# Kernel optimization log

Measured on AMD Instinct MI355X. Metric: run time of the kernel, lower is better.

## Reference

```python
import jax, jax.numpy as jnp
import numpy as np

EMB = 1024
FFN = 4096
H = 16
HD = EMB // H
EPS = 1e-6
SLOPE = 0.01


def leaky_relu(x):
    return jnp.where(x >= 0, x, SLOPE * x)


def layer_norm(x, g, b):
    mu = jnp.mean(x, axis=-1, keepdims=True)
    var = jnp.mean((x - mu) ** 2, axis=-1, keepdims=True)
    return (x - mu) * jax.lax.rsqrt(var + EPS) * g + b


def setup_inputs() -> dict:
    key = jax.random.key(0)
    ks = jax.random.split(key, 16)
    B, N = 2, 2048
    x = jax.random.normal(ks[0], (B, N, EMB), dtype=jnp.float32)

    def lin(k, fan_in, fan_out, kaiming_normal):
        kw, kb = jax.random.split(k)
        gain = float(np.sqrt(2.0 / (1.0 + SLOPE ** 2)))
        if kaiming_normal:
            W = jax.random.normal(kw, (fan_out, fan_in)) * (gain / np.sqrt(fan_in))
        else:
            bound = gain * np.sqrt(3.0 / fan_in)
            W = jax.random.uniform(kw, (fan_out, fan_in), minval=-bound, maxval=bound)
        b = jax.random.normal(kb, (fan_out,)) * 1e-6
        return W.astype(jnp.float32), b.astype(jnp.float32)

    Wq, bq = lin(ks[1], EMB, EMB, True)
    Wk, bk = lin(ks[2], EMB, EMB, True)
    Wv, bv = lin(ks[3], EMB, EMB, True)
    Wo, bo = lin(ks[4], EMB, EMB, True)
    W1, b1 = lin(ks[5], EMB, FFN, False)
    W2, b2 = lin(ks[6], FFN, EMB, False)
    return {
        "x": x,
        "ln1_g": jnp.ones((EMB,)), "ln1_b": jnp.zeros((EMB,)),
        "ln2_g": jnp.ones((EMB,)), "ln2_b": jnp.zeros((EMB,)),
        "Wq": Wq, "bq": bq, "Wk": Wk, "bk": bk, "Wv": Wv, "bv": bv,
        "Wo": Wo, "bo": bo, "W1": W1, "b1": b1, "W2": W2, "b2": b2,
    }


def reference(x, ln1_g, ln1_b, ln2_g, ln2_b, Wq, bq, Wk, bk, Wv, bv, Wo, bo, W1, b1, W2, b2):
    B, N, _ = x.shape
    h = x
    xn = layer_norm(x, ln1_g, ln1_b)
    # QKV projections, split heads: [B, H, N, HD]
    def heads(t):
        return t.reshape(B, N, H, HD).transpose(0, 2, 1, 3)
    q = heads(xn @ Wq.T + bq)
    k = heads(xn @ Wk.T + bk)
    v = heads(xn @ Wv.T + bv)
    scores = jnp.einsum('bhnd,bhmd->bhnm', q, k) / jnp.sqrt(jnp.float32(HD))
    probs = leaky_relu(scores)  # non-softmax attention
    ctx = jnp.einsum('bhnm,bhmd->bhnd', probs, v)
    ctx = ctx.transpose(0, 2, 1, 3).reshape(B, N, EMB)
    attn_out = ctx @ Wo.T + bo
    x = attn_out + h
    h = x
    xn = layer_norm(x, ln2_g, ln2_b)
    ff = leaky_relu(xn @ W1.T + b1) @ W2.T + b2
    return ff + h
```

## Files before the change

kernel.cpp:

```cpp
#include <hip/hip_runtime.h>
#include <hip/hip_bf16.h>


typedef unsigned short u16;
typedef unsigned int u32;
typedef __bf16 bf16x8 __attribute__((ext_vector_type(8)));
typedef __bf16 bf16x4 __attribute__((ext_vector_type(4)));
typedef float f32x4 __attribute__((ext_vector_type(4)));
typedef unsigned short u16x8 __attribute__((ext_vector_type(8)));
typedef unsigned int u32x2 __attribute__((ext_vector_type(2)));
typedef short s16x4 __attribute__((ext_vector_type(4)));

typedef const __attribute__((address_space(1))) void* as1cv;
typedef __attribute__((address_space(3))) void* as3v;

#define MFMA16(a, b, c) __builtin_amdgcn_mfma_f32_16x16x32_bf16((a), (b), (c), 0, 0, 0)
#define GLL16(g, l) __builtin_amdgcn_global_load_lds((as1cv)(g), (as3v)(l), 16, 0, 0)

__device__ __forceinline__ u16 f2bf(float f) {
  unsigned u = __builtin_bit_cast(unsigned, f);
  u += 0x7fffu + ((u >> 16) & 1u);
  return (u16)(u >> 16);
}
__device__ __forceinline__ float bf2f(u16 u) {
  return __builtin_bit_cast(float, ((unsigned)u) << 16);
}
__device__ __forceinline__ float lrelu(float v) { return fmaxf(v, 0.01f * v); }

__device__ __forceinline__ void mfma16x16(f32x4& c, bf16x4 a, bf16x4 b) {
#if __has_builtin(__builtin_amdgcn_mfma_f32_16x16x16bf16_1k)
  c = __builtin_amdgcn_mfma_f32_16x16x16bf16_1k(
      __builtin_bit_cast(s16x4, a), __builtin_bit_cast(s16x4, b), c, 0, 0, 0);
#else
  u32x2 au = __builtin_bit_cast(u32x2, a);
  u32x2 bu = __builtin_bit_cast(u32x2, b);
  asm volatile("s_nop 2\n\tv_mfma_f32_16x16x16_bf16 %0, %1, %2, %0"
               : "+v"(c) : "v"(au), "v"(bu));
#endif
}

__device__ __forceinline__ int xcds(int bid, int nwg) {
  int cpx = nwg >> 3;
  return (bid & 7) * cpx + (bid >> 3);
}

__global__ __launch_bounds__(256) void cvt6(
    const float* __restrict__ p0, const float* __restrict__ p1,
    const float* __restrict__ p2, const float* __restrict__ p3,
    const float* __restrict__ p4, const float* __restrict__ p5,
    u16* __restrict__ o0, u16* __restrict__ o1, u16* __restrict__ o2,
    u16* __restrict__ o3, u16* __restrict__ o4, u16* __restrict__ o5)
{
  int i = blockIdx.x * 256 + threadIdx.x;
  const float* src; u16* dst; int off;
  if (i < 4 * 131072) {
    int s = i >> 17; off = i & 131071;
    src = (s == 0) ? p0 : (s == 1) ? p1 : (s == 2) ? p2 : p3;
    dst = (s == 0) ? o0 : (s == 1) ? o1 : (s == 2) ? o2 : o3;
  } else {
    int j = i - 4 * 131072;
    int s = j >> 19; off = j & 524287;
    src = s ? p5 : p4;
    dst = s ? o5 : o4;
  }
  const float4* s4 = (const float4*)src;
  float4 a = s4[(size_t)off * 2], b = s4[(size_t)off * 2 + 1];
  u16x8 o = { f2bf(a.x), f2bf(a.y), f2bf(a.z), f2bf(a.w),
              f2bf(b.x), f2bf(b.y), f2bf(b.z), f2bf(b.w) };
  *(u16x8*)(dst + (size_t)off * 8) = o;
}

__global__ __launch_bounds__(256) void ln_k(
    const float* __restrict__ x, const float* __restrict__ g,
    const float* __restrict__ bb, u16* __restrict__ out)
{
  const int tid = threadIdx.x;
  const int row = blockIdx.x;
  const float4* xr = (const float4*)(x + (size_t)row * 1024);
  float4 v = xr[tid];
  float s  = v.x + v.y + v.z + v.w;
  float s2 = v.x*v.x + v.y*v.y + v.z*v.z + v.w*v.w;
#pragma unroll
  for (int o = 32; o > 0; o >>= 1) { s += __shfl_down(s, o, 64); s2 += __shfl_down(s2, o, 64); }
  __shared__ float sh[8];
  if ((tid & 63) == 0) { sh[tid >> 6] = s; sh[4 + (tid >> 6)] = s2; }
  __syncthreads();
  s  = sh[0] + sh[1] + sh[2] + sh[3];
  s2 = sh[4] + sh[5] + sh[6] + sh[7];
  float mu  = s * (1.0f / 1024.0f);
  float var = s2 * (1.0f / 1024.0f) - mu * mu;
  float rs  = rsqrtf(var + 1e-6f);
  float4 gv = ((const float4*)g)[tid];
  float4 bv = ((const float4*)bb)[tid];
  ushort4 o;
  o.x = f2bf((v.x - mu) * rs * gv.x + bv.x);
  o.y = f2bf((v.y - mu) * rs * gv.y + bv.y);
  o.z = f2bf((v.z - mu) * rs * gv.z + bv.z);
  o.w = f2bf((v.w - mu) * rs * gv.w + bv.w);
  ((ushort4*)out)[(size_t)row * 256 + tid] = o;
}

__device__ __forceinline__ void gemm_core128(
    const u16* __restrict__ A, const u16* __restrict__ W,
    int kstride, int klen,
    int row0, int wrow0, u16* lsA, u16* lsB, f32x4 (&acc)[4][4])
{
  const int tid  = threadIdx.x;
  const int lane = tid & 63, wave = tid >> 6;
  const int wr = wave >> 1, wc = wave & 1;
  const int lr = lane & 15, lg = lane >> 4;

  const u16* ga0 = A + (size_t)(row0 + (tid >> 2)) * kstride + (tid & 3) * 8;
  const u16* ga1 = ga0 + (size_t)64 * kstride;
  const u16* gb0 = W + (size_t)(wrow0 + (tid >> 2)) * kstride + (tid & 3) * 8;
  const u16* gb1 = gb0 + (size_t)64 * kstride;
  u16* la = lsA + tid * 8;
  u16* lb = lsB + tid * 8;

  GLL16(ga0, la); GLL16(ga1, la + 2048);
  GLL16(gb0, lb); GLL16(gb1, lb + 2048);
  ga0 += 32; ga1 += 32; gb0 += 32; gb1 += 32;
  __syncthreads();

  const int nsteps = klen >> 5;
  int cur = 0;
  for (int t = 0; t < nsteps; t++) {
    int nxt = cur ^ 1;
    if (t + 1 < nsteps) {
      GLL16(ga0, la + nxt * 4096);
      GLL16(ga1, la + nxt * 4096 + 2048);
      GLL16(gb0, lb + nxt * 4096);
      GLL16(gb1, lb + nxt * 4096 + 2048);
      ga0 += 32; ga1 += 32; gb0 += 32; gb1 += 32;
    }
    const u16* cA = lsA + cur * 4096;
    const u16* cB = lsB + cur * 4096;
    bf16x8 av[4], bv[4];
#pragma unroll
    for (int mi = 0; mi < 4; mi++)
      av[mi] = *reinterpret_cast<const bf16x8*>(cA + (wr * 64 + mi * 16 + lr) * 32 + lg * 8);
#pragma unroll
    for (int ni = 0; ni < 4; ni++)
      bv[ni] = *reinterpret_cast<const bf16x8*>(cB + (wc * 64 + ni * 16 + lr) * 32 + lg * 8);
#pragma unroll
    for (int mi = 0; mi < 4; mi++)
#pragma unroll
      for (int ni = 0; ni < 4; ni++)
        acc[mi][ni] = MFMA16(av[mi], bv[ni], acc[mi][ni]);
    __syncthreads();
    cur = nxt;
  }
}

__global__ __launch_bounds__(256, 4) void gemm_qkv(
    const u16* __restrict__ xn,
    const u16* __restrict__ Wq, const u16* __restrict__ Wk, const u16* __restrict__ Wv,
    const float* __restrict__ bq, const float* __restrict__ bk, const float* __restrict__ bv,
    u16* __restrict__ qb, u16* __restrict__ kb, u16* __restrict__ vtb)
{
  __shared__ u16 lsA[2 * 128 * 32];
  __shared__ u16 lsB[2 * 128 * 32];
  const int wid = xcds(blockIdx.x, 768);
  const int mt = wid / 24, nt = wid % 24;
  const int row0 = mt * 128, col0 = nt * 128;
  const int sel = col0 >> 10, c0 = col0 & 1023;
  const u16* W = (sel == 0) ? Wq : (sel == 1) ? Wk : Wv;
  const float* bias = (sel == 0) ? bq : (sel == 1) ? bk : bv;

  f32x4 acc[4][4];
  f32x4 z = {0.f, 0.f, 0.f, 0.f};
#pragma unroll
  for (int mi = 0; mi < 4; mi++)
#pragma unroll
    for (int ni = 0; ni < 4; ni++) acc[mi][ni] = z;

  gemm_core128(xn, W, 1024, 1024, row0, c0, lsA, lsB, acc);

  const int lane = threadIdx.x & 63, wave = threadIdx.x >> 6;
  const int wr = wave >> 1, wc = wave & 1;
  const int lr = lane & 15, lg = lane >> 4;
  const float qscale = (sel == 0) ? 0.125f : 1.0f;
#pragma unroll
  for (int ni = 0; ni < 4; ni++) {
    int c = c0 + wc * 64 + ni * 16 + lr;
    float bsv = bias[c];
    int h = c >> 6, hd = c & 63;
#pragma unroll
    for (int mi = 0; mi < 4; mi++) {
      int rbase = row0 + wr * 64 + mi * 16 + lg * 4;
      int b = rbase >> 11;
      int n = rbase & 2047;
      if (sel < 2) {
        u16* dst = (sel == 0) ? qb : kb;
        size_t base = ((size_t)(b * 16 + h) * 2048 + n) * 64 + hd;
#pragma unroll
        for (int r = 0; r < 4; r++)
          dst[base + (size_t)r * 64] = f2bf((acc[mi][ni][r] + bsv) * qscale);
      } else {
        size_t base = ((size_t)((b * 16 + h) * 64 + hd)) * 2048 + n;
        ushort4 o;
        o.x = f2bf(acc[mi][ni][0] + bsv);
        o.y = f2bf(acc[mi][ni][1] + bsv);
        o.z = f2bf(acc[mi][ni][2] + bsv);
        o.w = f2bf(acc[mi][ni][3] + bsv);
        *(ushort4*)(vtb + base) = o;
      }
    }
  }
}

template <int EPI>
__global__ __launch_bounds__(256, 4) void gemm128(
    const u16* __restrict__ A, const u16* __restrict__ W,
    const float* __restrict__ bias, float* __restrict__ outf,
    u16* __restrict__ outh, const float* __restrict__ extra,
    int K, int nTiles, int nwg)
{
  __shared__ u16 lsA[2 * 128 * 32];
  __shared__ u16 lsB[2 * 128 * 32];
  const int wid = xcds(blockIdx.x, nwg);
  const int mt = wid / nTiles, nt = wid % nTiles;
  const int row0 = mt * 128, col0 = nt * 128;

  f32x4 acc[4][4];
  f32x4 z = {0.f, 0.f, 0.f, 0.f};
#pragma unroll
  for (int mi = 0; mi < 4; mi++)
#pragma unroll
    for (int ni = 0; ni < 4; ni++) acc[mi][ni] = z;

  gemm_core128(A, W, K, K, row0, col0, lsA, lsB, acc);

  const int N = nTiles * 128;
  const int lane = threadIdx.x & 63, wave = threadIdx.x >> 6;
  const int wr = wave >> 1, wc = wave & 1;
  const int lr = lane & 15, lg = lane >> 4;
#pragma unroll
  for (int ni = 0; ni < 4; ni++) {
    int col = col0 + wc * 64 + ni * 16 + lr;
    float bsv = bias[col];
#pragma unroll
    for (int mi = 0; mi < 4; mi++) {
      int rbase = row0 + wr * 64 + mi * 16 + lg * 4;
#pragma unroll
      for (int r = 0; r < 4; r++) {
        float v = acc[mi][ni][r] + bsv;
        size_t idx = (size_t)(rbase + r) * N + col;
        if (EPI == 0) {
          outf[idx] = v + extra[idx];
        } else {
          outh[idx] = f2bf(lrelu(v));
        }
      }
    }
  }
}

__global__ __launch_bounds__(256, 4) void gemm_ffn2(
    const u16* __restrict__ A, const u16* __restrict__ W,
    u16* __restrict__ pout)
{
  __shared__ u16 lsA[2 * 128 * 32];
  __shared__ u16 lsB[2 * 128 * 32];
  const int wid = xcds(blockIdx.x, 1024);
  const int chunk = wid >> 8, rem = wid & 255;
  const int mt = rem >> 3, nt = rem & 7;
  const int row0 = mt * 128, col0 = nt * 128;

  f32x4 acc[4][4];
  f32x4 z = {0.f, 0.f, 0.f, 0.f};
#pragma unroll
  for (int mi = 0; mi < 4; mi++)
#pragma unroll
    for (int ni = 0; ni < 4; ni++) acc[mi][ni] = z;

  gemm_core128(A + chunk * 1024, W + chunk * 1024, 4096, 1024,
               row0, col0, lsA, lsB, acc);

  u16* out = pout + (size_t)chunk * (4096 * 1024);
  const int lane = threadIdx.x & 63, wave = threadIdx.x >> 6;
  const int wr = wave >> 1, wc = wave & 1;
  const int lr = lane & 15, lg = lane >> 4;
#pragma unroll
  for (int ni = 0; ni < 4; ni++) {
    int col = col0 + wc * 64 + ni * 16 + lr;
#pragma unroll
    for (int mi = 0; mi < 4; mi++) {
      int rbase = row0 + wr * 64 + mi * 16 + lg * 4;
#pragma unroll
      for (int r = 0; r < 4; r++)
        out[(size_t)(rbase + r) * 1024 + col] = f2bf(acc[mi][ni][r]);
    }
  }
}

__global__ __launch_bounds__(256) void reduce_ffn2(
    const u16* __restrict__ p, const float* __restrict__ b2,
    const float* __restrict__ x2, float* __restrict__ out)
{
  size_t i = ((size_t)blockIdx.x * 256 + threadIdx.x) * 4;
  int col = (int)(i & 1023);
  ushort4 a0 = *(const ushort4*)(p + i);
  ushort4 a1 = *(const ushort4*)(p + (size_t)(4096 * 1024) + i);
  ushort4 a2 = *(const ushort4*)(p + (size_t)(2 * 4096 * 1024) + i);
  ushort4 a3 = *(const ushort4*)(p + (size_t)(3 * 4096 * 1024) + i);
  float4 bv = *(const float4*)(b2 + col);
  float4 xv = *(const float4*)(x2 + i);
  float4 r;
  r.x = bf2f(a0.x) + bf2f(a1.x) + bf2f(a2.x) + bf2f(a3.x) + bv.x + xv.x;
  r.y = bf2f(a0.y) + bf2f(a1.y) + bf2f(a2.y) + bf2f(a3.y) + bv.y + xv.y;
  r.z = bf2f(a0.z) + bf2f(a1.z) + bf2f(a2.z) + bf2f(a3.z) + bv.z + xv.z;
  r.w = bf2f(a0.w) + bf2f(a1.w) + bf2f(a2.w) + bf2f(a3.w) + bv.w + xv.w;
  *(float4*)(out + i) = r;
}

__global__ __launch_bounds__(256, 2) void attn_k(
    const u16* __restrict__ qb, const u16* __restrict__ kb,
    const u16* __restrict__ vtb, u16* __restrict__ ctx)
{
  __shared__ u16 lds[4 * 8192];

  const int tid = threadIdx.x;
  const int lane = tid & 63, wq = tid >> 6;
  const int lr = lane & 15, lg = lane >> 4;
  const int wid = xcds(blockIdx.x, 512);
  const int bh = wid >> 4, qt = wid & 15;
  const int n0 = qt * 128;
  const u16* qh = qb + (size_t)bh * 2048 * 64;
  const u16* kh = kb + (size_t)bh * 2048 * 64;
  const u16* vh = vtb + (size_t)bh * 64 * 2048;

  const int srow = tid >> 3;
  const int sgg  = (tid & 7) ^ (srow & 7);
  const size_t koff0 = (size_t)srow * 64 + sgg * 8;
  const size_t koff1 = koff0 + (size_t)32 * 64;
  const size_t voff0 = (size_t)srow * 2048 + sgg * 8;
  const size_t voff1 = voff0 + (size_t)32 * 2048;
  const int dk0 = tid * 8, dk1 = tid * 8 + 2048;

#define STAGE_KV(t, jb)                                              \
  {                                                                  \
    const u16* ks_ = kh + (size_t)(t) * 4096;                        \
    const u16* vs_ = vh + (t) * 64;                                  \
    u16* lb_ = lds + (jb) * 8192;                                    \
    GLL16(ks_ + koff0, lb_ + dk0);                                   \
    GLL16(ks_ + koff1, lb_ + dk1);                                   \
    GLL16(vs_ + voff0, lb_ + 4096 + dk0);                            \
    GLL16(vs_ + voff1, lb_ + 4096 + dk1);                            \
  }

  STAGE_KV(0, 0);
  STAGE_KV(1, 1);

  bf16x8 qr[2][2];
#pragma unroll
  for (int qi = 0; qi < 2; qi++)
#pragma unroll
    for (int ks = 0; ks < 2; ks++)
      qr[qi][ks] = *(const bf16x8*)(
          qh + (size_t)(n0 + wq * 32 + qi * 16 + lr) * 64 + ks * 32 + lg * 8);
  asm volatile("" ::: "memory");

  f32x4 z = {0.f, 0.f, 0.f, 0.f};
  f32x4 cacc[4][2];
#pragma unroll
  for (int di = 0; di < 4; di++) { cacc[di][0] = z; cacc[di][1] = z; }

  const int lswz = lr & 7;
  for (int kt4 = 0; kt4 < 8; kt4++) {
#pragma unroll
    for (int j = 0; j < 4; j++) {
      const int t = kt4 * 4 + j;
      if (j == 3 && kt4 == 7) asm volatile("s_waitcnt vmcnt(0)" ::: "memory");
      else                    asm volatile("s_waitcnt vmcnt(4)" ::: "memory");
      __builtin_amdgcn_s_barrier();
      asm volatile("" ::: "memory");
      if (kt4 < 7 || j < 2) STAGE_KV(t + 2, (j + 2) & 3);

      const u16* lk = lds + j * 8192;
      const u16* lv = lds + j * 8192 + 4096;
#pragma unroll
      for (int ki = 0; ki < 4; ki++) {
        f32x4 s0 = z, s1 = z;
#pragma unroll
        for (int ks = 0; ks < 2; ks++) {
          bf16x8 kf = *(const bf16x8*)(
              lk + (ki * 16 + lr) * 64 + (((ks * 4 + lg) ^ lswz) * 8));
          s0 = MFMA16(kf, qr[0][ks], s0);
          s1 = MFMA16(kf, qr[1][ks], s1);
        }
        bf16x4 p0, p1;
#pragma unroll
        for (int r = 0; r < 4; r++) {
          p0[r] = (__bf16)lrelu(s0[r]);
          p1[r] = (__bf16)lrelu(s1[r]);
        }
#pragma unroll
        for (int di = 0; di < 4; di++) {
          bf16x4 vf = *(const bf16x4*)(
              lv + (di * 16 + lr) * 64 +
              (((ki * 2 + (lg >> 1)) ^ lswz) * 8) + (lg & 1) * 4);
          mfma16x16(cacc[di][0], vf, p0);
          mfma16x16(cacc[di][1], vf, p1);
        }
      }
    }
  }

  const int b = bh >> 4, h = bh & 15;
#pragma unroll
  for (int qi = 0; qi < 2; qi++) {
    int n = n0 + wq * 32 + qi * 16 + lr;
    u16* op = ctx + ((size_t)(b * 2048 + n)) * 1024 + h * 64;
#pragma unroll
    for (int di = 0; di < 4; di++) {
      ushort4 o;
      o.x = f2bf(cacc[di][qi][0]);
      o.y = f2bf(cacc[di][qi][1]);
      o.z = f2bf(cacc[di][qi][2]);
      o.w = f2bf(cacc[di][qi][3]);
      *(ushort4*)(op + di * 16 + lg * 4) = o;
    }
  }
#undef STAGE_KV
}

extern "C" void kernel_launch(void* const* d_in, const int* in_sizes, int n_in,
                              void* d_out, int out_size, void* d_ws, size_t ws_size,
                              hipStream_t stream) {
  (void)in_sizes; (void)n_in; (void)out_size; (void)ws_size;
  const float* x    = (const float*)d_in[0];
  const float* ln1g = (const float*)d_in[1];
  const float* ln1b = (const float*)d_in[2];
  const float* ln2g = (const float*)d_in[3];
  const float* ln2b = (const float*)d_in[4];
  const float* Wq = (const float*)d_in[5];  const float* bq = (const float*)d_in[6];
  const float* Wk = (const float*)d_in[7];  const float* bk = (const float*)d_in[8];
  const float* Wv = (const float*)d_in[9];  const float* bv = (const float*)d_in[10];
  const float* Wo = (const float*)d_in[11]; const float* bo = (const float*)d_in[12];
  const float* W1 = (const float*)d_in[13]; const float* b1 = (const float*)d_in[14];
  const float* W2 = (const float*)d_in[15]; const float* b2 = (const float*)d_in[16];

  char* ws = (char*)d_ws;
  u16*   WqB  = (u16*)(ws + ((size_t)0 << 20));
  u16*   WkB  = (u16*)(ws + ((size_t)2 << 20));
  u16*   WvB  = (u16*)(ws + ((size_t)4 << 20));
  u16*   WoB  = (u16*)(ws + ((size_t)6 << 20));
  u16*   W1B  = (u16*)(ws + ((size_t)8 << 20));
  u16*   W2B  = (u16*)(ws + ((size_t)16 << 20));
  u16*   xn1  = (u16*)(ws + ((size_t)24 << 20));
  u16*   qb   = (u16*)(ws + ((size_t)32 << 20));
  u16*   kb   = (u16*)(ws + ((size_t)40 << 20));
  u16*   vtb  = (u16*)(ws + ((size_t)48 << 20));
  u16*   ctxb = (u16*)(ws + ((size_t)56 << 20));
  float* x2   = (float*)(ws + ((size_t)64 << 20));
  u16*   xn2  = (u16*)(ws + ((size_t)80 << 20));
  u16*   ff1  = (u16*)(ws + ((size_t)88 << 20));
  u16*   pF2  = (u16*)(ws + ((size_t)24 << 20));

  dim3 blk(256);

  cvt6<<<dim3(6144), blk, 0, stream>>>(Wq, Wk, Wv, Wo, W1, W2,
                                       WqB, WkB, WvB, WoB, W1B, W2B);
  ln_k<<<dim3(4096), blk, 0, stream>>>(x, ln1g, ln1b, xn1);
  gemm_qkv<<<dim3(768), blk, 0, stream>>>(xn1, WqB, WkB, WvB, bq, bk, bv,
                                          qb, kb, vtb);
  attn_k<<<dim3(512), blk, 0, stream>>>(qb, kb, vtb, ctxb);
  gemm128<0><<<dim3(256), blk, 0, stream>>>(ctxb, WoB, bo, x2, (u16*)nullptr, x,
                                            1024, 8, 256);
  ln_k<<<dim3(4096), blk, 0, stream>>>(x2, ln2g, ln2b, xn2);
  gemm128<1><<<dim3(1024), blk, 0, stream>>>(xn2, W1B, b1, (float*)nullptr, ff1,
                                             (const float*)nullptr, 1024, 32, 1024);
  gemm_ffn2<<<dim3(1024), blk, 0, stream>>>(ff1, W2B, pF2);
  reduce_ffn2<<<dim3(4096), blk, 0, stream>>>(pF2, b2, x2, (float*)d_out);
}
```

Baseline: 353.4 us.

## Switch GEMM cores to 3-stage LDS pipeline and attention to 3-buffer ring

The shared GEMM core moves from double buffering with two __syncthreads per step to a three-buffer ring. It prefetches two K-steps ahead and waits with s_waitcnt vmcnt plus one barrier per step, so global loads overlap more compute. The attention kernel cuts its KV staging ring from four buffers to three, which lowers LDS use so three workgroups can fit per CU, and raises its launch bounds to match. GEMM launch bounds drop from 4 to 3 because of the larger LDS footprint. That can reduce GEMM occupancy, and the single-barrier ring depends on the wait counts being exactly right.

```diff
diff --git a/kernel.cpp b/kernel.cpp
--- a/kernel.cpp
+++ b/kernel.cpp
@@ -117,24 +117,29 @@
   u16* la = lsA + tid * 8;
   u16* lb = lsB + tid * 8;
 
-  GLL16(ga0, la); GLL16(ga1, la + 2048);
-  GLL16(gb0, lb); GLL16(gb1, lb + 2048);
-  ga0 += 32; ga1 += 32; gb0 += 32; gb1 += 32;
-  __syncthreads();
+#define GSTAGE(buf)                                                  \
+  {                                                                  \
+    GLL16(ga0, la + (buf) * 4096);                                   \
+    GLL16(ga1, la + (buf) * 4096 + 2048);                            \
+    GLL16(gb0, lb + (buf) * 4096);                                   \
+    GLL16(gb1, lb + (buf) * 4096 + 2048);                            \
+    ga0 += 32; ga1 += 32; gb0 += 32; gb1 += 32;                      \
+  }
 
   const int nsteps = klen >> 5;
-  int cur = 0;
+  GSTAGE(0); GSTAGE(1);
+
+  int bi = 0;
+  int bs = 2;
   for (int t = 0; t < nsteps; t++) {
-    int nxt = cur ^ 1;
-    if (t + 1 < nsteps) {
-      GLL16(ga0, la + nxt * 4096);
-      GLL16(ga1, la + nxt * 4096 + 2048);
-      GLL16(gb0, lb + nxt * 4096);
-      GLL16(gb1, lb + nxt * 4096 + 2048);
-      ga0 += 32; ga1 += 32; gb0 += 32; gb1 += 32;
-    }
-    const u16* cA = lsA + cur * 4096;
-    const u16* cB = lsB + cur * 4096;
+    if (t + 1 < nsteps) asm volatile("s_waitcnt vmcnt(4)" ::: "memory");
+    else                asm volatile("s_waitcnt vmcnt(0)" ::: "memory");
+    __builtin_amdgcn_s_barrier();
+    asm volatile("" ::: "memory");
+    if (t + 2 < nsteps) { GSTAGE(bs); bs = (bs == 2) ? 0 : bs + 1; }
+
+    const u16* cA = lsA + bi * 4096;
+    const u16* cB = lsB + bi * 4096;
     bf16x8 av[4], bv[4];
 #pragma unroll
     for (int mi = 0; mi < 4; mi++)
@@ -147,19 +152,19 @@
 #pragma unroll
       for (int ni = 0; ni < 4; ni++)
         acc[mi][ni] = MFMA16(av[mi], bv[ni], acc[mi][ni]);
-    __syncthreads();
-    cur = nxt;
-  }
-}
-
-__global__ __launch_bounds__(256, 4) void gemm_qkv(
+    bi = (bi == 2) ? 0 : bi + 1;
+  }
+#undef GSTAGE
+}
+
+__global__ __launch_bounds__(256, 3) void gemm_qkv(
     const u16* __restrict__ xn,
     const u16* __restrict__ Wq, const u16* __restrict__ Wk, const u16* __restrict__ Wv,
     const float* __restrict__ bq, const float* __restrict__ bk, const float* __restrict__ bv,
     u16* __restrict__ qb, u16* __restrict__ kb, u16* __restrict__ vtb)
 {
-  __shared__ u16 lsA[2 * 128 * 32];
-  __shared__ u16 lsB[2 * 128 * 32];
+  __shared__ u16 lsA[3 * 4096];
+  __shared__ u16 lsB[3 * 4096];
   const int wid = xcds(blockIdx.x, 768);
   const int mt = wid / 24, nt = wid % 24;
   const int row0 = mt * 128, col0 = nt * 128;
@@ -210,14 +215,14 @@
 }
 
 template <int EPI>
-__global__ __launch_bounds__(256, 4) void gemm128(
+__global__ __launch_bounds__(256, 3) void gemm128(
     const u16* __restrict__ A, const u16* __restrict__ W,
     const float* __restrict__ bias, float* __restrict__ outf,
     u16* __restrict__ outh, const float* __restrict__ extra,
     int K, int nTiles, int nwg)
 {
-  __shared__ u16 lsA[2 * 128 * 32];
-  __shared__ u16 lsB[2 * 128 * 32];
+  __shared__ u16 lsA[3 * 4096];
+  __shared__ u16 lsB[3 * 4096];
   const int wid = xcds(blockIdx.x, nwg);
   const int mt = wid / nTiles, nt = wid % nTiles;
   const int row0 = mt * 128, col0 = nt * 128;
@@ -256,12 +261,12 @@
   }
 }
 
-__global__ __launch_bounds__(256, 4) void gemm_ffn2(
+__global__ __launch_bounds__(256, 3) void gemm_ffn2(
     const u16* __restrict__ A, const u16* __restrict__ W,
     u16* __restrict__ pout)
 {
-  __shared__ u16 lsA[2 * 128 * 32];
-  __shared__ u16 lsB[2 * 128 * 32];
+  __shared__ u16 lsA[3 * 4096];
+  __shared__ u16 lsB[3 * 4096];
   const int wid = xcds(blockIdx.x, 1024);
   const int chunk = wid >> 8, rem = wid & 255;
   const int mt = rem >> 3, nt = rem & 7;
@@ -314,11 +319,11 @@
   *(float4*)(out + i) = r;
 }
 
-__global__ __launch_bounds__(256, 2) void attn_k(
+__global__ __launch_bounds__(256, 3) void attn_k(
     const u16* __restrict__ qb, const u16* __restrict__ kb,
     const u16* __restrict__ vtb, u16* __restrict__ ctx)
 {
-  __shared__ u16 lds[4 * 8192];
+  __shared__ u16 lds[3 * 8192];
 
   const int tid = threadIdx.x;
   const int lane = tid & 63, wq = tid >> 6;
@@ -367,44 +372,42 @@
   for (int di = 0; di < 4; di++) { cacc[di][0] = z; cacc[di][1] = z; }
 
   const int lswz = lr & 7;
-  for (int kt4 = 0; kt4 < 8; kt4++) {
-#pragma unroll
-    for (int j = 0; j < 4; j++) {
-      const int t = kt4 * 4 + j;
-      if (j == 3 && kt4 == 7) asm volatile("s_waitcnt vmcnt(0)" ::: "memory");
-      else                    asm volatile("s_waitcnt vmcnt(4)" ::: "memory");
-      __builtin_amdgcn_s_barrier();
-      asm volatile("" ::: "memory");
-      if (kt4 < 7 || j < 2) STAGE_KV(t + 2, (j + 2) & 3);
-
-      const u16* lk = lds + j * 8192;
-      const u16* lv = lds + j * 8192 + 4096;
-#pragma unroll
-      for (int ki = 0; ki < 4; ki++) {
-        f32x4 s0 = z, s1 = z;
-#pragma unroll
-        for (int ks = 0; ks < 2; ks++) {
-          bf16x8 kf = *(const bf16x8*)(
-              lk + (ki * 16 + lr) * 64 + (((ks * 4 + lg) ^ lswz) * 8));
-          s0 = MFMA16(kf, qr[0][ks], s0);
-          s1 = MFMA16(kf, qr[1][ks], s1);
-        }
-        bf16x4 p0, p1;
-#pragma unroll
-        for (int r = 0; r < 4; r++) {
-          p0[r] = (__bf16)lrelu(s0[r]);
-          p1[r] = (__bf16)lrelu(s1[r]);
-        }
-#pragma unroll
-        for (int di = 0; di < 4; di++) {
-          bf16x4 vf = *(const bf16x4*)(
-              lv + (di * 16 + lr) * 64 +
-              (((ki * 2 + (lg >> 1)) ^ lswz) * 8) + (lg & 1) * 4);
-          mfma16x16(cacc[di][0], vf, p0);
-          mfma16x16(cacc[di][1], vf, p1);
-        }
+  int bi = 0, bs = 2;
+  for (int t = 0; t < 32; t++) {
+    if (t < 31) asm volatile("s_waitcnt vmcnt(4)" ::: "memory");
+    else        asm volatile("s_waitcnt vmcnt(0)" ::: "memory");
+    __builtin_amdgcn_s_barrier();
+    asm volatile("" ::: "memory");
+    if (t + 2 < 32) { STAGE_KV(t + 2, bs); bs = (bs == 2) ? 0 : bs + 1; }
+
+    const u16* lk = lds + bi * 8192;
+    const u16* lv = lds + bi * 8192 + 4096;
+#pragma unroll
+    for (int ki = 0; ki < 4; ki++) {
+      f32x4 s0 = z, s1 = z;
+#pragma unroll
+      for (int ks = 0; ks < 2; ks++) {
+        bf16x8 kf = *(const bf16x8*)(
+            lk + (ki * 16 + lr) * 64 + (((ks * 4 + lg) ^ lswz) * 8));
+        s0 = MFMA16(kf, qr[0][ks], s0);
+        s1 = MFMA16(kf, qr[1][ks], s1);
+      }
+      bf16x4 p0, p1;
+#pragma unroll
+      for (int r = 0; r < 4; r++) {
+        p0[r] = (__bf16)lrelu(s0[r]);
+        p1[r] = (__bf16)lrelu(s1[r]);
+      }
+#pragma unroll
+      for (int di = 0; di < 4; di++) {
+        bf16x4 vf = *(const bf16x4*)(
+            lv + (di * 16 + lr) * 64 +
+            (((ki * 2 + (lg >> 1)) ^ lswz) * 8) + (lg & 1) * 4);
+        mfma16x16(cacc[di][0], vf, p0);
+        mfma16x16(cacc[di][1], vf, p1);
       }
     }
+    bi = (bi == 2) ? 0 : bi + 1;
   }
 
   const int b = bh >> 4, h = bh & 15;
```

After: 353.8 us. About the same (+0.1%).
